# Optimization experiments

Hardware: AMD Instinct MI355X
Metric: run time of the kernel (lower is better)

Reference implementation:

```python
import jax, jax.numpy as jnp
import numpy as np

LP, LQ, B, D = 4096, 4096, 32, 512  # lp, lq, batch, hidden (=in_size1=in_size2)
WSCALE = 0.04  # ~ torch Linear default uniform bound 1/sqrt(512)


def setup_inputs() -> dict:
    key = jax.random.key(0)
    ks = jax.random.split(key, 11)
    return {
        "h": jax.random.normal(ks[0], (LP, B, D), jnp.float32),
        "u": jax.random.normal(ks[1], (B, LQ, D), jnp.float32),
        "v": jax.random.normal(ks[2], (B, D, 1), jnp.float32),
        "Wu_w": jax.random.normal(ks[3], (D, D), jnp.float32) * WSCALE,
        "Wu_b": jax.random.normal(ks[4], (D,), jnp.float32) * WSCALE,
        "Wh_w": jax.random.normal(ks[5], (D, D), jnp.float32) * WSCALE,
        "Wha_w": jax.random.normal(ks[6], (D, D), jnp.float32) * WSCALE,
        "W_ih": jax.random.normal(ks[7], (3 * D, D), jnp.float32) * WSCALE,
        "W_hh": jax.random.normal(ks[8], (3 * D, D), jnp.float32) * WSCALE,
        "b_ih": jax.random.normal(ks[9], (3 * D,), jnp.float32) * WSCALE,
        "b_hh": jax.random.normal(ks[10], (3 * D,), jnp.float32) * WSCALE,
    }


def _gru_cell(x, hprev, W_ih, W_hh, b_ih, b_hh):
    # torch GRUCell semantics
    gi = x @ W_ih.T + b_ih          # [B, 3D]
    gh = hprev @ W_hh.T + b_hh      # [B, 3D]
    i_r, i_z, i_n = jnp.split(gi, 3, axis=-1)
    h_r, h_z, h_n = jnp.split(gh, 3, axis=-1)
    r = jax.nn.sigmoid(i_r + h_r)
    z = jax.nn.sigmoid(i_z + h_z)
    n = jnp.tanh(i_n + r * h_n)
    return (1.0 - z) * n + z * hprev


def reference(h, u, v, Wu_w, Wu_b, Wh_w, Wha_w, W_ih, W_hh, b_ih, b_hh):
    # h: [lp, B, d1], u: [B, lq, d2], v: [B, H, 1]
    vb = v[:, :, 0]  # [B, H]
    # --- attention over u ---
    xq = jnp.tanh(jnp.einsum('bqd,hd->bqh', u, Wu_w) + Wu_b)   # [B, lq, H]
    s = jnp.einsum('bqh,bh->bq', xq, vb)                        # bmm(x, v).squeeze
    a = jax.nn.softmax(s, axis=1)
    r = jnp.einsum('bq,bqd->bd', a, u)                          # [B, d2]
    # --- attention over h conditioned on r, twice with GRU update in between ---
    Whh_proj = jnp.einsum('pbd,hd->pbh', h, Wh_w)               # [lp, B, H] (reused)

    def h_attn(rvec):
        x = jnp.tanh(Whh_proj + (rvec @ Wha_w.T)[None])         # [lp, B, H]
        s = jnp.einsum('pbh,bh->bp', x, vb)                     # [B, lp]
        return jax.nn.softmax(s, axis=1)

    p1 = h_attn(r)
    c = jnp.einsum('bp,pbd->bd', p1, h)                         # [B, d1]
    r2 = _gru_cell(c, r, W_ih, W_hh, b_ih, b_hh)                # [B, d2]
    p2 = h_attn(r2)
    return (p1, p2)
```

## Files before the change

### kernel.cpp

```cpp
#include <hip/hip_runtime.h>
#include <hip/hip_bf16.h>

typedef __attribute__((ext_vector_type(4))) float f4;
typedef __attribute__((ext_vector_type(8))) _Float16 h8;
typedef __attribute__((ext_vector_type(4))) _Float16 h4;

#define MTOT 131072

__device__ __forceinline__ float fast_tanh(float x){
    float e = exp2f(x * 2.8853900817779268f);
    return 1.0f - 2.0f * __builtin_amdgcn_rcpf(e + 1.0f);
}
__device__ __forceinline__ float fast_sigmoid(float x){
    return __builtin_amdgcn_rcpf(1.0f + exp2f(-x * 1.4426950408889634f));
}
__device__ __forceinline__ float wave_reduce_sum(float v){
    #pragma unroll
    for (int off = 32; off; off >>= 1) v += __shfl_down(v, off, 64);
    return v;
}

__device__ __forceinline__ void gl_lds16(const void* g, void* l){
    __builtin_amdgcn_global_load_lds(
        (const __attribute__((address_space(1))) void*)g,
        (__attribute__((address_space(3))) void*)l, 16, 0, 0);
}

__global__ __launch_bounds__(256) void k_pack_both(
    const float* __restrict__ Wu, const float* __restrict__ Wh,
    _Float16* __restrict__ Pu, _Float16* __restrict__ Ph)
{
    const int g = blockIdx.x;
    const float* W = (g < 128) ? Wu : Wh;
    _Float16*    P = (g < 128) ? Pu : Ph;
    const int idx = (g & 127) * 4 + (threadIdx.x >> 6);
    const int l = threadIdx.x & 63;
    const int n = (idx >> 4) * 16 + (l & 15);
    const int k = (idx & 15) * 32 + (l >> 4) * 8;
    const float* src = W + n * 512 + k;
    f4 s0 = *(const f4*)(src);
    f4 s1 = *(const f4*)(src + 4);
    h8 v;
    #pragma unroll
    for (int i = 0; i < 4; i++){ v[i] = (_Float16)s0[i]; v[4+i] = (_Float16)s1[i]; }
    *(h8*)(P + (idx << 9) + l * 8) = v;
}

union SMem {
    struct { float A[3][4096]; _Float16 W[3][8192]; } st;
    _Float16 ep[64][264];
};

template<int MODE>
__global__ __launch_bounds__(512) void k_score_gemm(
    const float* __restrict__ A,
    const _Float16* __restrict__ Wp,
    const float* __restrict__ vb,
    const float* __restrict__ addvec,
    float* __restrict__ spart,
    _Float16* __restrict__ whh)
{
    __shared__ __align__(16) SMem sm;

    const int tid  = threadIdx.x;
    const int lane = tid & 63;
    const int wv   = tid >> 6;
    const int wr   = wv >> 2;
    const int wc   = wv & 3;
    const int mt   = blockIdx.x >> 1;
    const int nc   = blockIdx.x & 1;
    const int m0   = mt * 128;
    const int n0   = nc * 256;

    const int lr = lane & 15;
    const int kq = lane >> 4;

    const int arow0 = tid >> 3;
    const int aseg  = tid & 7;

    auto stage = [&](int kt, int buf){
        #pragma unroll
        for (int i = 0; i < 2; i++){
            const int row = arow0 + i*64;
            const int sg  = aseg ^ (row & 7);
            const float* g = A + (long)(m0 + row)*512 + kt*32 + sg*4;
            char* l = (char*)&sm.st.A[0][0] + buf*16384 + (i*512 + wv*64)*16;
            gl_lds16(g, l);
        }
        #pragma unroll
        for (int i = 0; i < 2; i++){
            const int chunk = i*8 + wv;
            const _Float16* g = Wp + ((long)((nc*16 + chunk)*16 + kt))*512 + lane*8;
            char* l = (char*)&sm.st.W[0][0] + buf*16384 + chunk*1024;
            gl_lds16(g, l);
        }
    };

    f4 acc[4][4] = {};

    stage(0, 0); stage(1, 1); stage(2, 2);
    __builtin_amdgcn_sched_barrier(0);

    const int plo = (2*kq)     ^ (lr & 7);
    const int phi = (2*kq + 1) ^ (lr & 7);

    #pragma unroll
    for (int kt = 0; kt < 16; ++kt){
        const int buf = kt % 3;
        if (kt < 14)       asm volatile("s_waitcnt vmcnt(8)" ::: "memory");
        else if (kt == 14) asm volatile("s_waitcnt vmcnt(4)" ::: "memory");
        else               asm volatile("s_waitcnt vmcnt(0)" ::: "memory");
        __builtin_amdgcn_s_barrier();
        __builtin_amdgcn_sched_barrier(0);

        const float* Ab = &sm.st.A[0][0] + buf*4096;
        h8 af[4];
        #pragma unroll
        for (int mi = 0; mi < 4; mi++){
            const int row = wr*64 + mi*16 + lr;
            f4 lo = *(const f4*)(Ab + row*32 + plo*4);
            f4 hi = *(const f4*)(Ab + row*32 + phi*4);
            h8 v;
            #pragma unroll
            for (int i = 0; i < 4; i++){ v[i] = (_Float16)lo[i]; v[4+i] = (_Float16)hi[i]; }
            af[mi] = v;
        }
        const _Float16* Wb = &sm.st.W[0][0] + buf*8192;
        h8 bf[4];
        #pragma unroll
        for (int ni = 0; ni < 4; ni++)
            bf[ni] = *(const h8*)(Wb + (wc*4 + ni)*512 + lane*8);

        asm volatile("s_waitcnt lgkmcnt(0)" ::: "memory");
        __builtin_amdgcn_sched_barrier(0);
        __builtin_amdgcn_s_barrier();
        __builtin_amdgcn_sched_barrier(0);

        if (kt < 13) stage(kt + 3, buf);

        __builtin_amdgcn_s_setprio(1);
        #pragma unroll
        for (int mi = 0; mi < 4; mi++)
            #pragma unroll
            for (int ni = 0; ni < 4; ni++)
                acc[mi][ni] = __builtin_amdgcn_mfma_f32_16x16x32_f16(af[mi], bf[ni], acc[mi][ni], 0, 0, 0);
        __builtin_amdgcn_s_setprio(0);
    }
    __builtin_amdgcn_sched_barrier(0);
    __syncthreads();

    const int jrow = (lane >> 4) * 4;
    for (int hf = 0; hf < 2; ++hf){
        if (wr == hf){
            #pragma unroll
            for (int mi = 0; mi < 4; mi++)
                #pragma unroll
                for (int ni = 0; ni < 4; ni++)
                    #pragma unroll
                    for (int j = 0; j < 4; j++)
                        sm.ep[mi*16 + jrow + j][wc*64 + ni*16 + lr] = (_Float16)acc[mi][ni][j];
        }
        __syncthreads();

        if (MODE == 1 && whh){
            const int row = tid >> 3, seg = tid & 7;
            const int m = m0 + hf*64 + row;
            const _Float16* esrc = &sm.ep[row][seg*32];
            _Float16* gdst = whh + (long)m*512 + n0 + seg*32;
            #pragma unroll
            for (int i = 0; i < 4; i++)
                *(h8*)(gdst + i*8) = *(const h8*)(esrc + i*8);
        }

        #pragma unroll
        for (int rr = 0; rr < 8; ++rr){
            const int erow = wv*8 + rr;
            const int m = m0 + hf*64 + erow;
            const int b = (MODE == 0) ? (m >> 12) : (m & 31);
            const int n = n0 + lane*4;
            h4 hv = *(const h4*)&sm.ep[erow][lane*4];
            f4 vbv = *(const f4*)&vb[b*512 + n];
            f4 adv;
            if (MODE == 0) adv = *(const f4*)&addvec[n];
            else           adv = *(const f4*)&addvec[b*512 + n];
            float p = 0.f;
            #pragma unroll
            for (int i = 0; i < 4; i++)
                p += fast_tanh((float)hv[i] + adv[i]) * vbv[i];
            p = wave_reduce_sum(p);
            if (lane == 0){
                const int sIdx = (MODE == 0) ? m : (((m & 31) << 12) | (m >> 5));
                spart[nc*MTOT + sIdx] = p;
            }
        }
        __syncthreads();
    }
}

__global__ __launch_bounds__(256) void k_softmax(const float* __restrict__ s0,
        const float* __restrict__ s1, float* __restrict__ out)
{
    __shared__ float red[8];
    __shared__ float bcast[2];
    const int b = blockIdx.x, t = threadIdx.x;
    const int wv = t >> 6, lane = t & 63;
    const float* p0 = s0 + b*4096;
    const float* p1 = s1 ? s1 + b*4096 : nullptr;
    float vals[16];
    float mx = -3.0e38f;
    #pragma unroll
    for (int i = 0; i < 16; i++){
        float v = p0[t + i*256];
        if (p1) v += p1[t + i*256];
        vals[i] = v;
        mx = fmaxf(mx, v);
    }
    #pragma unroll
    for (int off = 32; off; off >>= 1) mx = fmaxf(mx, __shfl_down(mx, off, 64));
    if (lane == 0) red[wv] = mx;
    __syncthreads();
    if (t == 0) bcast[0] = fmaxf(fmaxf(red[0], red[1]), fmaxf(red[2], red[3]));
    __syncthreads();
    const float gmax = bcast[0];
    float sum = 0.f;
    #pragma unroll
    for (int i = 0; i < 16; i++){
        vals[i] = exp2f((vals[i] - gmax) * 1.4426950408889634f);
        sum += vals[i];
    }
    sum = wave_reduce_sum(sum);
    if (lane == 0) red[wv] = sum;
    __syncthreads();
    if (t == 0) bcast[1] = red[0] + red[1] + red[2] + red[3];
    __syncthreads();
    const float inv = 1.0f / bcast[1];
    #pragma unroll
    for (int i = 0; i < 16; i++) out[b*4096 + t + i*256] = vals[i] * inv;
}

__global__ __launch_bounds__(512) void k_weighted_rowsum(
    const float* __restrict__ wts, const float* __restrict__ X,
    float* __restrict__ part, int mode)
{
    const int b = blockIdx.x, ch = blockIdx.y, d = threadIdx.x;
    float acc = 0.f;
    const int q0 = ch * 128;
    for (int q = q0; q < q0 + 128; ++q){
        const float w = wts[b*4096 + q];
        if (fabsf(w) > 1e-20f){
            const float* xp = (mode == 0) ? (X + ((long)(b*4096 + q) * 512) + d)
                                          : (X + ((long)(q*32 + b) * 512) + d);
            acc += w * xp[0];
        }
    }
    part[(ch*32 + b)*512 + d] = acc;
}

__global__ void k_reduce_part(const float* __restrict__ part, float* __restrict__ out){
    const int b = blockIdx.x, d = threadIdx.x;
    float s = 0.f;
    #pragma unroll
    for (int ch = 0; ch < 32; ++ch) s += part[(ch*32 + b)*512 + d];
    out[b*512 + d] = s;
}

__global__ __launch_bounds__(256) void k_matvec(
    const float* __restrict__ W, const float* __restrict__ x,
    const float* __restrict__ bias, float* __restrict__ out, int N)
{
    __shared__ float xs[512];
    const int b = blockIdx.x, t = threadIdx.x;
    xs[t] = x[b*512 + t];
    xs[t + 256] = x[b*512 + 256 + t];
    __syncthreads();
    const int wv = t >> 6, lane = t & 63;
    f4 x0 = *(const f4*)&xs[lane*8];
    f4 x1 = *(const f4*)&xs[lane*8 + 4];
    const int rbase = blockIdx.y*32 + wv*8;
    for (int rr = 0; rr < 8; ++rr){
        const int row = rbase + rr;
        const float* wp = W + (long)row*512 + lane*8;
        f4 w0 = *(const f4*)wp;
        f4 w1 = *(const f4*)(wp + 4);
        float p = w0[0]*x0[0] + w0[1]*x0[1] + w0[2]*x0[2] + w0[3]*x0[3]
                + w1[0]*x1[0] + w1[1]*x1[1] + w1[2]*x1[2] + w1[3]*x1[3];
        p = wave_reduce_sum(p);
        if (lane == 0) out[b*N + row] = p + (bias ? bias[row] : 0.f);
    }
}

__global__ void k_gru(const float* __restrict__ gi, const float* __restrict__ gh,
                      const float* __restrict__ r, float* __restrict__ r2)
{
    const int b = blockIdx.x, d = threadIdx.x;
    const float* gib = gi + b*1536;
    const float* ghb = gh + b*1536;
    const float rg = fast_sigmoid(gib[d]        + ghb[d]);
    const float z  = fast_sigmoid(gib[512 + d]  + ghb[512 + d]);
    const float n  = fast_tanh   (gib[1024 + d] + rg * ghb[1024 + d]);
    r2[b*512 + d] = (1.f - z)*n + z*r[b*512 + d];
}

__global__ __launch_bounds__(256) void k_t2(const _Float16* __restrict__ whh,
        const float* __restrict__ vb, const float* __restrict__ ra2, float* __restrict__ t2)
{
    const int wv = threadIdx.x >> 6, lane = threadIdx.x & 63;
    const int mbase = blockIdx.x*32 + wv*8;
    for (int rr = 0; rr < 8; ++rr){
        const int m = mbase + rr;
        const int b = m & 31;
        h8 hv = *(const h8*)(whh + (long)m*512 + lane*8);
        const float* rp  = ra2 + b*512 + lane*8;
        const float* vbp = vb  + b*512 + lane*8;
        float p = 0.f;
        #pragma unroll
        for (int i = 0; i < 8; i++)
            p += fast_tanh((float)hv[i] + rp[i]) * vbp[i];
        p = wave_reduce_sum(p);
        if (lane == 0) t2[((m & 31) << 12) | (m >> 5)] = p;
    }
}

extern "C" void kernel_launch(void* const* d_in, const int* in_sizes, int n_in,
                              void* d_out, int out_size, void* d_ws, size_t ws_size,
                              hipStream_t stream)
{
    const float* h_    = (const float*)d_in[0];
    const float* u_    = (const float*)d_in[1];
    const float* vb    = (const float*)d_in[2];
    const float* Wu_w  = (const float*)d_in[3];
    const float* Wu_b  = (const float*)d_in[4];
    const float* Wh_w  = (const float*)d_in[5];
    const float* Wha_w = (const float*)d_in[6];
    const float* W_ih  = (const float*)d_in[7];
    const float* W_hh  = (const float*)d_in[8];
    const float* b_ih  = (const float*)d_in[9];
    const float* b_hh  = (const float*)d_in[10];
    float* out = (float*)d_out;

    char* ws = (char*)d_ws;
    float*    spart = (float*)(ws + 0);
    float*    tpart = (float*)(ws + 1048576);
    float*    a_    = (float*)(ws + 2097152);
    _Float16* Wpu   = (_Float16*)(ws + 2621440);
    _Float16* Wph   = (_Float16*)(ws + 3145728);
    float*    r_    = (float*)(ws + 3670016);
    float*    ra1   = (float*)(ws + 3735552);
    float*    c_    = (float*)(ws + 3801088);
    float*    r2    = (float*)(ws + 3866624);
    float*    ra2   = (float*)(ws + 3932160);
    float*    gi    = (float*)(ws + 3997696);
    float*    gh    = (float*)(ws + 4194304);
    float*    part  = (float*)(ws + 4390912);
    _Float16* whh   = (_Float16*)(ws + 8388608);
    const bool big = ws_size >= (size_t)8388608 + (size_t)MTOT * 512 * 2;

    k_pack_both<<<256, 256, 0, stream>>>(Wu_w, Wh_w, Wpu, Wph);

    k_score_gemm<0><<<2048, 512, 0, stream>>>(u_, Wpu, vb, Wu_b, spart, nullptr);
    k_softmax<<<32, 256, 0, stream>>>(spart, spart + MTOT, a_);
    k_weighted_rowsum<<<dim3(32, 32), 512, 0, stream>>>(a_, u_, part, 0);
    k_reduce_part<<<32, 512, 0, stream>>>(part, r_);
    k_matvec<<<dim3(32, 16), 256, 0, stream>>>(Wha_w, r_, nullptr, ra1, 512);

    k_score_gemm<1><<<2048, 512, 0, stream>>>(h_, Wph, vb, ra1, tpart, big ? whh : nullptr);
    k_softmax<<<32, 256, 0, stream>>>(tpart, tpart + MTOT, out);

    k_weighted_rowsum<<<dim3(32, 32), 512, 0, stream>>>(out, h_, part, 1);
    k_reduce_part<<<32, 512, 0, stream>>>(part, c_);
    k_matvec<<<dim3(32, 48), 256, 0, stream>>>(W_ih, c_, b_ih, gi, 1536);
    k_matvec<<<dim3(32, 48), 256, 0, stream>>>(W_hh, r_, b_hh, gh, 1536);
    k_gru<<<32, 512, 0, stream>>>(gi, gh, r_, r2);
    k_matvec<<<dim3(32, 16), 256, 0, stream>>>(Wha_w, r2, nullptr, ra2, 512);

    if (big){
        k_t2<<<4096, 256, 0, stream>>>(whh, vb, ra2, tpart);
        k_softmax<<<32, 256, 0, stream>>>(tpart, nullptr, out + MTOT);
    } else {
        k_score_gemm<2><<<2048, 512, 0, stream>>>(h_, Wph, vb, ra2, tpart, nullptr);
        k_softmax<<<32, 256, 0, stream>>>(tpart, tpart + MTOT, out + MTOT);
    }
}
```

Baseline: 593.0 us.

## Stage A through registers as fp16 in LDS and read weights directly from global

New measurement: 754.3 us. 1.27x slower.

```diff
diff --git a/kernel.cpp b/kernel.cpp
--- a/kernel.cpp
+++ b/kernel.cpp
@@ -4,6 +4,7 @@
 typedef __attribute__((ext_vector_type(4))) float f4;
 typedef __attribute__((ext_vector_type(8))) _Float16 h8;
 typedef __attribute__((ext_vector_type(4))) _Float16 h4;
+typedef __attribute__((ext_vector_type(2))) __fp16 hp2;
 
 #define MTOT 131072
 
@@ -18,12 +19,6 @@
     #pragma unroll
     for (int off = 32; off; off >>= 1) v += __shfl_down(v, off, 64);
     return v;
-}
-
-__device__ __forceinline__ void gl_lds16(const void* g, void* l){
-    __builtin_amdgcn_global_load_lds(
-        (const __attribute__((address_space(1))) void*)g,
-        (__attribute__((address_space(3))) void*)l, 16, 0, 0);
 }
 
 __global__ __launch_bounds__(256) void k_pack_both(
@@ -46,13 +41,14 @@
     *(h8*)(P + (idx << 9) + l * 8) = v;
 }
 
-union SMem {
-    struct { float A[3][4096]; _Float16 W[3][8192]; } st;
+union SMemG {
+    _Float16 A[2][128][32];
     _Float16 ep[64][264];
 };
+union HU { h8 v; hp2 p[4]; };
 
 template<int MODE>
-__global__ __launch_bounds__(512) void k_score_gemm(
+__global__ __launch_bounds__(512, 4) void k_score_gemm(
     const float* __restrict__ A,
     const _Float16* __restrict__ Wp,
     const float* __restrict__ vb,
@@ -60,7 +56,7 @@
     float* __restrict__ spart,
     _Float16* __restrict__ whh)
 {
-    __shared__ __align__(16) SMem sm;
+    __shared__ __align__(16) SMemG sm;
 
     const int tid  = threadIdx.x;
     const int lane = tid & 63;
@@ -75,68 +71,52 @@
     const int lr = lane & 15;
     const int kq = lane >> 4;
 
-    const int arow0 = tid >> 3;
-    const int aseg  = tid & 7;
-
-    auto stage = [&](int kt, int buf){
-        #pragma unroll
-        for (int i = 0; i < 2; i++){
-            const int row = arow0 + i*64;
-            const int sg  = aseg ^ (row & 7);
-            const float* g = A + (long)(m0 + row)*512 + kt*32 + sg*4;
-            char* l = (char*)&sm.st.A[0][0] + buf*16384 + (i*512 + wv*64)*16;
-            gl_lds16(g, l);
-        }
-        #pragma unroll
-        for (int i = 0; i < 2; i++){
-            const int chunk = i*8 + wv;
-            const _Float16* g = Wp + ((long)((nc*16 + chunk)*16 + kt))*512 + lane*8;
-            char* l = (char*)&sm.st.W[0][0] + buf*16384 + chunk*1024;
-            gl_lds16(g, l);
-        }
+    const int srow = tid >> 2;
+    const int sg   = tid & 3;
+    const int sgp  = sg ^ ((srow >> 1) & 3);
+    const float* agbase = A + (long)(m0 + srow) * 512 + sg * 8;
+    _Float16* swr = &sm.A[0][0][0] + srow * 32 + sgp * 8;
+
+    const _Float16* wbase = Wp + (nc * 16 + wc * 4) * 16 * 512 + lane * 8;
+
+    f4 apf[3][2];
+    auto issueA = [&](int kt){
+        const float* p = agbase + kt * 32;
+        apf[kt % 3][0] = *(const f4*)p;
+        apf[kt % 3][1] = *(const f4*)(p + 4);
     };
+    auto writeA = [&](int kt){
+        HU u;
+        u.p[0] = __builtin_amdgcn_cvt_pkrtz(apf[kt % 3][0][0], apf[kt % 3][0][1]);
+        u.p[1] = __builtin_amdgcn_cvt_pkrtz(apf[kt % 3][0][2], apf[kt % 3][0][3]);
+        u.p[2] = __builtin_amdgcn_cvt_pkrtz(apf[kt % 3][1][0], apf[kt % 3][1][1]);
+        u.p[3] = __builtin_amdgcn_cvt_pkrtz(apf[kt % 3][1][2], apf[kt % 3][1][3]);
+        *(h8*)(swr + (kt & 1) * 4096) = u.v;
+    };
+
+    issueA(0); issueA(1); issueA(2);
+    writeA(0);
+    __syncthreads();
 
     f4 acc[4][4] = {};
 
-    stage(0, 0); stage(1, 1); stage(2, 2);
-    __builtin_amdgcn_sched_barrier(0);
-
-    const int plo = (2*kq)     ^ (lr & 7);
-    const int phi = (2*kq + 1) ^ (lr & 7);
-
     #pragma unroll
     for (int kt = 0; kt < 16; ++kt){
-        const int buf = kt % 3;
-        if (kt < 14)       asm volatile("s_waitcnt vmcnt(8)" ::: "memory");
-        else if (kt == 14) asm volatile("s_waitcnt vmcnt(4)" ::: "memory");
-        else               asm volatile("s_waitcnt vmcnt(0)" ::: "memory");
-        __builtin_amdgcn_s_barrier();
-        __builtin_amdgcn_sched_barrier(0);
-
-        const float* Ab = &sm.st.A[0][0] + buf*4096;
+        const int cur = kt & 1;
         h8 af[4];
         #pragma unroll
         for (int mi = 0; mi < 4; mi++){
             const int row = wr*64 + mi*16 + lr;
-            f4 lo = *(const f4*)(Ab + row*32 + plo*4);
-            f4 hi = *(const f4*)(Ab + row*32 + phi*4);
-            h8 v;
-            #pragma unroll
-            for (int i = 0; i < 4; i++){ v[i] = (_Float16)lo[i]; v[4+i] = (_Float16)hi[i]; }
-            af[mi] = v;
-        }
-        const _Float16* Wb = &sm.st.W[0][0] + buf*8192;
+            const int gp  = kq ^ ((row >> 1) & 3);
+            af[mi] = *(const h8*)(&sm.A[cur][0][0] + row * 32 + gp * 8);
+        }
         h8 bf[4];
         #pragma unroll
         for (int ni = 0; ni < 4; ni++)
-            bf[ni] = *(const h8*)(Wb + (wc*4 + ni)*512 + lane*8);
-
-        asm volatile("s_waitcnt lgkmcnt(0)" ::: "memory");
-        __builtin_amdgcn_sched_barrier(0);
-        __builtin_amdgcn_s_barrier();
-        __builtin_amdgcn_sched_barrier(0);
-
-        if (kt < 13) stage(kt + 3, buf);
+            bf[ni] = *(const h8*)(wbase + (ni * 16 + kt) * 512);
+
+        if (kt < 15)     writeA(kt + 1);
+        if (kt + 3 < 16) issueA(kt + 3);
 
         __builtin_amdgcn_s_setprio(1);
         #pragma unroll
@@ -145,8 +125,12 @@
             for (int ni = 0; ni < 4; ni++)
                 acc[mi][ni] = __builtin_amdgcn_mfma_f32_16x16x32_f16(af[mi], bf[ni], acc[mi][ni], 0, 0, 0);
         __builtin_amdgcn_s_setprio(0);
-    }
-    __builtin_amdgcn_sched_barrier(0);
+
+        asm volatile("s_waitcnt lgkmcnt(0)" ::: "memory");
+        __builtin_amdgcn_sched_barrier(0);
+        __builtin_amdgcn_s_barrier();
+        __builtin_amdgcn_sched_barrier(0);
+    }
     __syncthreads();
 
     const int jrow = (lane >> 4) * 4;
```

## Retile score GEMM to 128x128 tiles with double buffering and block swizzle

Applied to the files above, without the earlier changes.

Measured after the change: 815.3 us. 1.37x slower.

```diff
diff --git a/kernel.cpp b/kernel.cpp
--- a/kernel.cpp
+++ b/kernel.cpp
@@ -2,6 +2,7 @@
 #include <hip/hip_bf16.h>
 
 typedef __attribute__((ext_vector_type(4))) float f4;
+typedef __attribute__((ext_vector_type(2))) float f2;
 typedef __attribute__((ext_vector_type(8))) _Float16 h8;
 typedef __attribute__((ext_vector_type(4))) _Float16 h4;
 
@@ -46,13 +47,13 @@
     *(h8*)(P + (idx << 9) + l * 8) = v;
 }
 
-union SMem {
-    struct { float A[3][4096]; _Float16 W[3][8192]; } st;
-    _Float16 ep[64][264];
+union SMemG {
+    struct { float A[2][128][32]; _Float16 W[2][128][32]; } st;
+    _Float16 ep[64][136];
 };
 
 template<int MODE>
-__global__ __launch_bounds__(512) void k_score_gemm(
+__global__ __launch_bounds__(256) void k_score_gemm(
     const float* __restrict__ A,
     const _Float16* __restrict__ Wp,
     const float* __restrict__ vb,
@@ -60,83 +61,67 @@
     float* __restrict__ spart,
     _Float16* __restrict__ whh)
 {
-    __shared__ __align__(16) SMem sm;
+    __shared__ __align__(16) SMemG sm;
 
     const int tid  = threadIdx.x;
     const int lane = tid & 63;
     const int wv   = tid >> 6;
-    const int wr   = wv >> 2;
-    const int wc   = wv & 3;
-    const int mt   = blockIdx.x >> 1;
-    const int nc   = blockIdx.x & 1;
+    const int wr   = wv >> 1;
+    const int wc   = wv & 1;
+    const int swz  = ((blockIdx.x & 7) << 9) | (blockIdx.x >> 3);
+    const int mt   = swz >> 2;
+    const int nc   = swz & 3;
     const int m0   = mt * 128;
-    const int n0   = nc * 256;
+    const int n0   = nc * 128;
 
     const int lr = lane & 15;
     const int kq = lane >> 4;
 
-    const int arow0 = tid >> 3;
-    const int aseg  = tid & 7;
-
     auto stage = [&](int kt, int buf){
         #pragma unroll
+        for (int i = 0; i < 4; i++){
+            const int row = (wv*4 + i)*8 + (lane >> 3);
+            const int sg  = (lane & 7) ^ (row & 7);
+            const float* g = A + (long)(m0 + row)*512 + kt*32 + sg*4;
+            char* l = (char*)&sm.st.A[buf][0][0] + (wv*4 + i)*1024;
+            gl_lds16(g, l);
+        }
+        #pragma unroll
         for (int i = 0; i < 2; i++){
-            const int row = arow0 + i*64;
-            const int sg  = aseg ^ (row & 7);
-            const float* g = A + (long)(m0 + row)*512 + kt*32 + sg*4;
-            char* l = (char*)&sm.st.A[0][0] + buf*16384 + (i*512 + wv*64)*16;
+            const int c = i*4 + wv;
+            const _Float16* g = Wp + ((long)((nc*8 + c)*16 + kt))*512 + lane*8;
+            char* l = (char*)&sm.st.W[buf][0][0] + c*1024;
             gl_lds16(g, l);
         }
-        #pragma unroll
-        for (int i = 0; i < 2; i++){
-            const int chunk = i*8 + wv;
-            const _Float16* g = Wp + ((long)((nc*16 + chunk)*16 + kt))*512 + lane*8;
-            char* l = (char*)&sm.st.W[0][0] + buf*16384 + chunk*1024;
-            gl_lds16(g, l);
-        }
     };
 
     f4 acc[4][4] = {};
 
-    stage(0, 0); stage(1, 1); stage(2, 2);
-    __builtin_amdgcn_sched_barrier(0);
-
-    const int plo = (2*kq)     ^ (lr & 7);
-    const int phi = (2*kq + 1) ^ (lr & 7);
+    stage(0, 0);
+    __syncthreads();
 
     #pragma unroll
     for (int kt = 0; kt < 16; ++kt){
-        const int buf = kt % 3;
-        if (kt < 14)       asm volatile("s_waitcnt vmcnt(8)" ::: "memory");
-        else if (kt == 14) asm volatile("s_waitcnt vmcnt(4)" ::: "memory");
-        else               asm volatile("s_waitcnt vmcnt(0)" ::: "memory");
-        __builtin_amdgcn_s_barrier();
-        __builtin_amdgcn_sched_barrier(0);
-
-        const float* Ab = &sm.st.A[0][0] + buf*4096;
+        const int buf = kt & 1;
+        if (kt < 15) stage(kt + 1, buf ^ 1);
+
+        const float* Ab = &sm.st.A[buf][0][0];
         h8 af[4];
         #pragma unroll
         for (int mi = 0; mi < 4; mi++){
             const int row = wr*64 + mi*16 + lr;
-            f4 lo = *(const f4*)(Ab + row*32 + plo*4);
-            f4 hi = *(const f4*)(Ab + row*32 + phi*4);
+            f4 lo = *(const f4*)(Ab + row*32 + ((2*kq)     ^ (row & 7))*4);
+            f4 hi = *(const f4*)(Ab + row*32 + ((2*kq + 1) ^ (row & 7))*4);
             h8 v;
             #pragma unroll
             for (int i = 0; i < 4; i++){ v[i] = (_Float16)lo[i]; v[4+i] = (_Float16)hi[i]; }
             af[mi] = v;
         }
-        const _Float16* Wb = &sm.st.W[0][0] + buf*8192;
+        const _Float16* Wb = &sm.st.W[buf][0][0];
         h8 bf[4];
         #pragma unroll
         for (int ni = 0; ni < 4; ni++)
             bf[ni] = *(const h8*)(Wb + (wc*4 + ni)*512 + lane*8);
-
-        asm volatile("s_waitcnt lgkmcnt(0)" ::: "memory");
-        __builtin_amdgcn_sched_barrier(0);
-        __builtin_amdgcn_s_barrier();
-        __builtin_amdgcn_sched_barrier(0);
-
-        if (kt < 13) stage(kt + 3, buf);
 
         __builtin_amdgcn_s_setprio(1);
         #pragma unroll
@@ -145,11 +130,11 @@
             for (int ni = 0; ni < 4; ni++)
                 acc[mi][ni] = __builtin_amdgcn_mfma_f32_16x16x32_f16(af[mi], bf[ni], acc[mi][ni], 0, 0, 0);
         __builtin_amdgcn_s_setprio(0);
-    }
-    __builtin_amdgcn_sched_barrier(0);
-    __syncthreads();
-
-    const int jrow = (lane >> 4) * 4;
+
+        __syncthreads();
+    }
+
+    const int jrow = kq * 4;
     for (int hf = 0; hf < 2; ++hf){
         if (wr == hf){
             #pragma unroll
@@ -163,7 +148,7 @@
         __syncthreads();
 
         if (MODE == 1 && whh){
-            const int row = tid >> 3, seg = tid & 7;
+            const int row = tid >> 2, seg = tid & 3;
             const int m = m0 + hf*64 + row;
             const _Float16* esrc = &sm.ep[row][seg*32];
             _Float16* gdst = whh + (long)m*512 + n0 + seg*32;
@@ -173,20 +158,18 @@
         }
 
         #pragma unroll
-        for (int rr = 0; rr < 8; ++rr){
-            const int erow = wv*8 + rr;
+        for (int rr = 0; rr < 16; ++rr){
+            const int erow = wv*16 + rr;
             const int m = m0 + hf*64 + erow;
             const int b = (MODE == 0) ? (m >> 12) : (m & 31);
-            const int n = n0 + lane*4;
-            h4 hv = *(const h4*)&sm.ep[erow][lane*4];
-            f4 vbv = *(const f4*)&vb[b*512 + n];
-            f4 adv;
-            if (MODE == 0) adv = *(const f4*)&addvec[n];
-            else           adv = *(const f4*)&addvec[b*512 + n];
-            float p = 0.f;
-            #pragma unroll
-            for (int i = 0; i < 4; i++)
-                p += fast_tanh((float)hv[i] + adv[i]) * vbv[i];
+            const int n = n0 + lane*2;
+            const float e0 = (float)sm.ep[erow][lane*2];
+            const float e1 = (float)sm.ep[erow][lane*2 + 1];
+            f2 vbv = *(const f2*)&vb[b*512 + n];
+            f2 adv;
+            if (MODE == 0) adv = *(const f2*)&addvec[n];
+            else           adv = *(const f2*)&addvec[b*512 + n];
+            float p = fast_tanh(e0 + adv[0]) * vbv[0] + fast_tanh(e1 + adv[1]) * vbv[1];
             p = wave_reduce_sum(p);
             if (lane == 0){
                 const int sIdx = (MODE == 0) ? m : (((m & 31) << 12) | (m >> 5));
@@ -197,21 +180,19 @@
     }
 }
 
-__global__ __launch_bounds__(256) void k_softmax(const float* __restrict__ s0,
-        const float* __restrict__ s1, float* __restrict__ out)
+__global__ __launch_bounds__(256) void k_softmax(const float* __restrict__ s,
+        int npart, float* __restrict__ out)
 {
     __shared__ float red[8];
     __shared__ float bcast[2];
     const int b = blockIdx.x, t = threadIdx.x;
     const int wv = t >> 6, lane = t & 63;
-    const float* p0 = s0 + b*4096;
-    const float* p1 = s1 ? s1 + b*4096 : nullptr;
     float vals[16];
     float mx = -3.0e38f;
     #pragma unroll
     for (int i = 0; i < 16; i++){
-        float v = p0[t + i*256];
-        if (p1) v += p1[t + i*256];
+        float v = s[b*4096 + t + i*256];
+        for (int p = 1; p < npart; p++) v += s[p*MTOT + b*4096 + t + i*256];
         vals[i] = v;
         mx = fmaxf(mx, v);
     }
@@ -244,8 +225,8 @@
 {
     const int b = blockIdx.x, ch = blockIdx.y, d = threadIdx.x;
     float acc = 0.f;
-    const int q0 = ch * 128;
-    for (int q = q0; q < q0 + 128; ++q){
+    const int q0 = ch * 256;
+    for (int q = q0; q < q0 + 256; ++q){
         const float w = wts[b*4096 + q];
         if (fabsf(w) > 1e-20f){
             const float* xp = (mode == 0) ? (X + ((long)(b*4096 + q) * 512) + d)
@@ -260,7 +241,7 @@
     const int b = blockIdx.x, d = threadIdx.x;
     float s = 0.f;
     #pragma unroll
-    for (int ch = 0; ch < 32; ++ch) s += part[(ch*32 + b)*512 + d];
+    for (int ch = 0; ch < 16; ++ch) s += part[(ch*32 + b)*512 + d];
     out[b*512 + d] = s;
 }
 
@@ -340,33 +321,33 @@
 
     char* ws = (char*)d_ws;
     float*    spart = (float*)(ws + 0);
-    float*    tpart = (float*)(ws + 1048576);
-    float*    a_    = (float*)(ws + 2097152);
-    _Float16* Wpu   = (_Float16*)(ws + 2621440);
-    _Float16* Wph   = (_Float16*)(ws + 3145728);
-    float*    r_    = (float*)(ws + 3670016);
-    float*    ra1   = (float*)(ws + 3735552);
-    float*    c_    = (float*)(ws + 3801088);
-    float*    r2    = (float*)(ws + 3866624);
-    float*    ra2   = (float*)(ws + 3932160);
-    float*    gi    = (float*)(ws + 3997696);
-    float*    gh    = (float*)(ws + 4194304);
-    float*    part  = (float*)(ws + 4390912);
+    float*    tpart = (float*)(ws + 2097152);
+    float*    a_    = (float*)(ws + 4194304);
+    _Float16* Wpu   = (_Float16*)(ws + 4718592);
+    _Float16* Wph   = (_Float16*)(ws + 5242880);
+    float*    r_    = (float*)(ws + 5767168);
+    float*    ra1   = (float*)(ws + 5832704);
+    float*    c_    = (float*)(ws + 5898240);
+    float*    r2    = (float*)(ws + 5963776);
+    float*    ra2   = (float*)(ws + 6029312);
+    float*    gi    = (float*)(ws + 6094848);
+    float*    gh    = (float*)(ws + 6291456);
+    float*    part  = (float*)(ws + 6488064);
     _Float16* whh   = (_Float16*)(ws + 8388608);
     const bool big = ws_size >= (size_t)8388608 + (size_t)MTOT * 512 * 2;
 
     k_pack_both<<<256, 256, 0, stream>>>(Wu_w, Wh_w, Wpu, Wph);
 
-    k_score_gemm<0><<<2048, 512, 0, stream>>>(u_, Wpu, vb, Wu_b, spart, nullptr);
-    k_softmax<<<32, 256, 0, stream>>>(spart, spart + MTOT, a_);
-    k_weighted_rowsum<<<dim3(32, 32), 512, 0, stream>>>(a_, u_, part, 0);
+    k_score_gemm<0><<<4096, 256, 0, stream>>>(u_, Wpu, vb, Wu_b, spart, nullptr);
+    k_softmax<<<32, 256, 0, stream>>>(spart, 4, a_);
+    k_weighted_rowsum<<<dim3(32, 16), 512, 0, stream>>>(a_, u_, part, 0);
     k_reduce_part<<<32, 512, 0, stream>>>(part, r_);
     k_matvec<<<dim3(32, 16), 256, 0, stream>>>(Wha_w, r_, nullptr, ra1, 512);
 
-    k_score_gemm<1><<<2048, 512, 0, stream>>>(h_, Wph, vb, ra1, tpart, big ? whh : nullptr);
-    k_softmax<<<32, 256, 0, stream>>>(tpart, tpart + MTOT, out);
-
-    k_weighted_rowsum<<<dim3(32, 32), 512, 0, stream>>>(out, h_, part, 1);
+    k_score_gemm<1><<<4096, 256, 0, stream>>>(h_, Wph, vb, ra1, tpart, big ? whh : nullptr);
+    k_softmax<<<32, 256, 0, stream>>>(tpart, 4, out);
+
+    k_weighted_rowsum<<<dim3(32, 16), 512, 0, stream>>>(out, h_, part, 1);
     k_reduce_part<<<32, 512, 0, stream>>>(part, c_);
     k_matvec<<<dim3(32, 48), 256, 0, stream>>>(W_ih, c_, b_ih, gi, 1536);
     k_matvec<<<dim3(32, 48), 256, 0, stream>>>(W_hh, r_, b_hh, gh, 1536);
@@ -375,9 +356,9 @@
 
     if (big){
         k_t2<<<4096, 256, 0, stream>>>(whh, vb, ra2, tpart);
-        k_softmax<<<32, 256, 0, stream>>>(tpart, nullptr, out + MTOT);
+        k_softmax<<<32, 256, 0, stream>>>(tpart, 1, out + MTOT);
     } else {
-        k_score_gemm<2><<<2048, 512, 0, stream>>>(h_, Wph, vb, ra2, tpart, nullptr);
-        k_softmax<<<32, 256, 0, stream>>>(tpart, tpart + MTOT, out + MTOT);
-    }
-}
+        k_score_gemm<2><<<4096, 256, 0, stream>>>(h_, Wph, vb, ra2, tpart, nullptr);
+        k_softmax<<<32, 256, 0, stream>>>(tpart, 4, out + MTOT);
+    }
+}
```

## Simplify score GEMM to double-buffered pipeline with XCD block swizzle

Applied to the files above, without the earlier changes.

After: 523.7 us. -11.7%, faster.

```diff
diff --git a/kernel.cpp b/kernel.cpp
--- a/kernel.cpp
+++ b/kernel.cpp
@@ -47,7 +47,7 @@
 }
 
 union SMem {
-    struct { float A[3][4096]; _Float16 W[3][8192]; } st;
+    struct { float A[2][4096]; _Float16 W[2][8192]; } st;
     _Float16 ep[64][264];
 };
 
@@ -67,8 +67,9 @@
     const int wv   = tid >> 6;
     const int wr   = wv >> 2;
     const int wc   = wv & 3;
-    const int mt   = blockIdx.x >> 1;
-    const int nc   = blockIdx.x & 1;
+    const int swz  = ((blockIdx.x & 7) << 8) | (blockIdx.x >> 3);
+    const int mt   = swz >> 1;
+    const int nc   = swz & 1;
     const int m0   = mt * 128;
     const int n0   = nc * 256;
 
@@ -98,20 +99,15 @@
 
     f4 acc[4][4] = {};
 
-    stage(0, 0); stage(1, 1); stage(2, 2);
-    __builtin_amdgcn_sched_barrier(0);
+    stage(0, 0);
+    __syncthreads();
 
     const int plo = (2*kq)     ^ (lr & 7);
     const int phi = (2*kq + 1) ^ (lr & 7);
 
-    #pragma unroll
     for (int kt = 0; kt < 16; ++kt){
-        const int buf = kt % 3;
-        if (kt < 14)       asm volatile("s_waitcnt vmcnt(8)" ::: "memory");
-        else if (kt == 14) asm volatile("s_waitcnt vmcnt(4)" ::: "memory");
-        else               asm volatile("s_waitcnt vmcnt(0)" ::: "memory");
-        __builtin_amdgcn_s_barrier();
-        __builtin_amdgcn_sched_barrier(0);
+        const int buf = kt & 1;
+        if (kt < 15) stage(kt + 1, buf ^ 1);
 
         const float* Ab = &sm.st.A[0][0] + buf*4096;
         h8 af[4];
@@ -131,23 +127,14 @@
         for (int ni = 0; ni < 4; ni++)
             bf[ni] = *(const h8*)(Wb + (wc*4 + ni)*512 + lane*8);
 
-        asm volatile("s_waitcnt lgkmcnt(0)" ::: "memory");
-        __builtin_amdgcn_sched_barrier(0);
-        __builtin_amdgcn_s_barrier();
-        __builtin_amdgcn_sched_barrier(0);
-
-        if (kt < 13) stage(kt + 3, buf);
-
-        __builtin_amdgcn_s_setprio(1);
         #pragma unroll
         for (int mi = 0; mi < 4; mi++)
             #pragma unroll
             for (int ni = 0; ni < 4; ni++)
                 acc[mi][ni] = __builtin_amdgcn_mfma_f32_16x16x32_f16(af[mi], bf[ni], acc[mi][ni], 0, 0, 0);
-        __builtin_amdgcn_s_setprio(0);
-    }
-    __builtin_amdgcn_sched_barrier(0);
-    __syncthreads();
+
+        __syncthreads();
+    }
 
     const int jrow = (lane >> 4) * 4;
     for (int hf = 0; hf < 2; ++hf){
@@ -197,21 +184,21 @@
     }
 }
 
-__global__ __launch_bounds__(256) void k_softmax(const float* __restrict__ s0,
-        const float* __restrict__ s1, float* __restrict__ out)
+template<int NP>
+__global__ __launch_bounds__(256) void k_softmax(const float* __restrict__ s,
+        float* __restrict__ out)
 {
     __shared__ float red[8];
     __shared__ float bcast[2];
     const int b = blockIdx.x, t = threadIdx.x;
     const int wv = t >> 6, lane = t & 63;
-    const float* p0 = s0 + b*4096;
-    const float* p1 = s1 ? s1 + b*4096 : nullptr;
     float vals[16];
     float mx = -3.0e38f;
     #pragma unroll
     for (int i = 0; i < 16; i++){
-        float v = p0[t + i*256];
-        if (p1) v += p1[t + i*256];
+        float v = s[b*4096 + t + i*256];
+        #pragma unroll
+        for (int p = 1; p < NP; p++) v += s[p*MTOT + b*4096 + t + i*256];
         vals[i] = v;
         mx = fmaxf(mx, v);
     }
@@ -341,30 +328,30 @@
     char* ws = (char*)d_ws;
     float*    spart = (float*)(ws + 0);
     float*    tpart = (float*)(ws + 1048576);
-    float*    a_    = (float*)(ws + 2097152);
-    _Float16* Wpu   = (_Float16*)(ws + 2621440);
-    _Float16* Wph   = (_Float16*)(ws + 3145728);
-    float*    r_    = (float*)(ws + 3670016);
-    float*    ra1   = (float*)(ws + 3735552);
-    float*    c_    = (float*)(ws + 3801088);
-    float*    r2    = (float*)(ws + 3866624);
-    float*    ra2   = (float*)(ws + 3932160);
-    float*    gi    = (float*)(ws + 3997696);
-    float*    gh    = (float*)(ws + 4194304);
-    float*    part  = (float*)(ws + 4390912);
+    float*    part  = (float*)(ws + 2097152);
+    float*    a_    = (float*)(ws + 4194304);
+    _Float16* Wpu   = (_Float16*)(ws + 4718592);
+    _Float16* Wph   = (_Float16*)(ws + 5242880);
+    float*    r_    = (float*)(ws + 5767168);
+    float*    ra1   = (float*)(ws + 5832704);
+    float*    c_    = (float*)(ws + 5898240);
+    float*    r2    = (float*)(ws + 5963776);
+    float*    ra2   = (float*)(ws + 6029312);
+    float*    gi    = (float*)(ws + 6094848);
+    float*    gh    = (float*)(ws + 6291456);
     _Float16* whh   = (_Float16*)(ws + 8388608);
     const bool big = ws_size >= (size_t)8388608 + (size_t)MTOT * 512 * 2;
 
     k_pack_both<<<256, 256, 0, stream>>>(Wu_w, Wh_w, Wpu, Wph);
 
     k_score_gemm<0><<<2048, 512, 0, stream>>>(u_, Wpu, vb, Wu_b, spart, nullptr);
-    k_softmax<<<32, 256, 0, stream>>>(spart, spart + MTOT, a_);
+    k_softmax<2><<<32, 256, 0, stream>>>(spart, a_);
     k_weighted_rowsum<<<dim3(32, 32), 512, 0, stream>>>(a_, u_, part, 0);
     k_reduce_part<<<32, 512, 0, stream>>>(part, r_);
     k_matvec<<<dim3(32, 16), 256, 0, stream>>>(Wha_w, r_, nullptr, ra1, 512);
 
     k_score_gemm<1><<<2048, 512, 0, stream>>>(h_, Wph, vb, ra1, tpart, big ? whh : nullptr);
-    k_softmax<<<32, 256, 0, stream>>>(tpart, tpart + MTOT, out);
+    k_softmax<2><<<32, 256, 0, stream>>>(tpart, out);
 
     k_weighted_rowsum<<<dim3(32, 32), 512, 0, stream>>>(out, h_, part, 1);
     k_reduce_part<<<32, 512, 0, stream>>>(part, c_);
@@ -375,9 +362,9 @@
 
     if (big){
         k_t2<<<4096, 256, 0, stream>>>(whh, vb, ra2, tpart);
-        k_softmax<<<32, 256, 0, stream>>>(tpart, nullptr, out + MTOT);
+        k_softmax<1><<<32, 256, 0, stream>>>(tpart, out + MTOT);
     } else {
         k_score_gemm<2><<<2048, 512, 0, stream>>>(h_, Wph, vb, ra2, tpart, nullptr);
-        k_softmax<<<32, 256, 0, stream>>>(tpart, tpart + MTOT, out + MTOT);
-    }
-}
+        k_softmax<2><<<32, 256, 0, stream>>>(tpart, out + MTOT);
+    }
+}
```
